# Optimization experiments

Hardware: AMD Instinct MI355X
Metric: run time of the kernel (lower is better)

The kernel has to match this reference:

```python
import jax, jax.numpy as jnp
import numpy as np

B, N = 4, 1024
IN_FEAT = 64
FNET = 64          # code requires fnet_feat == in_feat
OUT_FEAT = 64
RANK = 16
ST1 = 16
ST2 = 16
MIN_NN = 16


def _roll_idx(n_rolls, stride, F):
    # myroll(h, shift) == roll right by `shift` (mod F). Shifts used: 0, then (ss+1)*stride for ss=1..n_rolls-1.
    shifts = np.array([0] + [(ss + 1) * stride for ss in range(1, n_rolls)])
    j = np.arange(F)
    return jnp.asarray((j[None, :] - shifts[:, None]) % F)  # [n_rolls, F]


def setup_inputs() -> dict:
    key = jax.random.key(0)
    ks = jax.random.split(key, 10)
    h = jax.random.normal(ks[0], (B, N, IN_FEAT), jnp.float32)
    D = jax.random.uniform(ks[1], (B, N, N), jnp.float32)
    W0 = jax.random.normal(ks[2], (IN_FEAT, FNET), jnp.float32) * (1.0 / np.sqrt(IN_FEAT))
    b0 = jax.random.normal(ks[3], (1, FNET), jnp.float32) * 0.02
    W1 = jax.random.normal(ks[4], (FNET, ST1 * RANK), jnp.float32) * (1.0 / (np.sqrt(FNET) * np.sqrt(IN_FEAT)))
    b1 = jax.random.normal(ks[5], (1, RANK, IN_FEAT), jnp.float32) * 0.02
    W2 = jax.random.normal(ks[6], (FNET, ST2 * RANK), jnp.float32) * (1.0 / (np.sqrt(FNET) * np.sqrt(IN_FEAT)))
    b2 = jax.random.normal(ks[7], (1, RANK, OUT_FEAT), jnp.float32) * 0.02
    Wl = jax.random.normal(ks[8], (FNET, RANK), jnp.float32) * (1.0 / np.sqrt(RANK))
    bl = jax.random.normal(ks[9], (1, RANK), jnp.float32) * 0.02
    return {"h": h, "D": D, "W0": W0, "b0": b0, "W1": W1, "b1": b1,
            "W2": W2, "b2": b2, "Wl": Wl, "bl": bl}


def reference(h, D, W0, b0, W1, b1, W2, b2, Wl, bl):
    Bb, Nn, f = h.shape
    # k+1 nearest (smallest D): index 0 is the closest ('self'), 1..k are the neighbors
    _, top_idx = jax.lax.top_k(-D, MIN_NN + 1)            # [B, N, K+1]
    top_idx2 = jnp.repeat(top_idx[:, :, 0], MIN_NN, axis=1)  # [B, N*K] (repeat_interleave)
    nbr = top_idx[:, :, 1:].reshape(Bb, Nn * MIN_NN)         # [B, N*K]
    xt1 = jnp.take_along_axis(h, nbr[:, :, None], axis=1)    # [B, N*K, f]
    xt2 = jnp.take_along_axis(h, top_idx2[:, :, None], axis=1)
    labels = (xt1 - xt2).reshape(-1, f)                      # [E, f], E = B*N*K
    x1 = xt1.reshape(-1, f)
    d_labels = jnp.sum(labels * labels, axis=1).reshape(-1, MIN_NN)  # [B*N, K]
    lab = jax.nn.leaky_relu(labels @ W0 + b0, negative_slope=0.02)   # [E, FNET]
    E = lab.shape[0]
    idx1 = _roll_idx(IN_FEAT // ST1, ST1, FNET)
    idx2 = _roll_idx(OUT_FEAT // ST2, ST2, FNET)
    # per-edge weight generation via rolled copies of lab
    theta1 = (lab[:, idx1].reshape(-1, FNET) @ W1).reshape(E, RANK, IN_FEAT) + b1   # [E, R, in]
    theta2 = (lab[:, idx2].reshape(-1, FNET) @ W2).reshape(E, RANK, OUT_FEAT) + b2  # [E, R, out]
    thetal = lab @ Wl + bl                                                          # [E, R]
    x = jnp.einsum('erf,ef->er', theta1, x1) * thetal      # [E, R]
    x = jnp.einsum('ero,er->eo', theta2, x)                # [E, out]
    x = x.reshape(-1, MIN_NN, OUT_FEAT) * jnp.exp(-d_labels / 10.0)[:, :, None]
    x = jnp.sum(x, axis=1).reshape(-1, OUT_FEAT, Nn)       # faithful to torch .reshape(-1, out, N)
    return x
```

## Files before the change

kernel.cpp:

```cpp
#include <hip/hip_runtime.h>
#include <math.h>

#define NN 1024
#define K 16

typedef _Float16 f16;
typedef f16 f16x8 __attribute__((ext_vector_type(8)));
typedef float f32x4 __attribute__((ext_vector_type(4)));

typedef __attribute__((address_space(1))) void gvoid;
typedef __attribute__((address_space(3))) void svoid;

#define W0F_OFF 0
#define W1F_OFF 8192
#define W2F_OFF 40960
#define WLF_OFF 73728
#define B1F_OFF 75776
#define FRAG_BYTES 77824

#define MFMA16(a,b,c) __builtin_amdgcn_mfma_f32_16x16x32_f16((a),(b),(c),0,0,0)

template<int CTRL>
__device__ __forceinline__ float dppf(float v) {
    return __int_as_float(__builtin_amdgcn_update_dpp(0, __float_as_int(v), CTRL, 0xF, 0xF, true));
}
template<int CTRL>
__device__ __forceinline__ int dppi(int v) {
    return __builtin_amdgcn_update_dpp(0, v, CTRL, 0xF, 0xF, true);
}
__device__ __forceinline__ float rowsum16(float v) {
    v += dppf<0xB1>(v);
    v += dppf<0x4E>(v);
    v += dppf<0x124>(v);
    v += dppf<0x128>(v);
    return v;
}
__device__ __forceinline__ void argmin_step(float& bv, int& bidx, float ov, int oi) {
    bool t = (ov < bv) || (ov == bv && oi < bidx);
    bv = t ? ov : bv;
    bidx = t ? oi : bidx;
}

__global__ __launch_bounds__(256) void pre_kernel(const float* __restrict__ D,
                                                  const float* __restrict__ W0,
                                                  const float* __restrict__ W1,
                                                  const float* __restrict__ W2,
                                                  const float* __restrict__ Wl,
                                                  const float* __restrict__ b1,
                                                  int* __restrict__ selfIdx,
                                                  int* __restrict__ nbrIdx,
                                                  f16* __restrict__ frag) {
    if (blockIdx.x >= 1024) {
        int c = (blockIdx.x - 1024) * 256 + threadIdx.x;
        if (c >= 76 * 64) return;
        int fg   = c >> 6;
        int lane = c & 63;
        int lrow = lane & 15;
        int kgrp = lane >> 4;
        float src[8];
        if (fg < 8) {
            int kt = fg >> 2, nt = fg & 3;
            int n = nt * 16 + lrow;
#pragma unroll
            for (int i = 0; i < 8; ++i) src[i] = W0[(kt * 32 + kgrp * 8 + i) * 64 + n];
        } else if (fg < 40) {
            int t = fg - 8;
            int q = t >> 3, kt = (t >> 2) & 1, nt = t & 3;
            int f = nt * 16 + lrow;
#pragma unroll
            for (int i = 0; i < 8; ++i) src[i] = W1[f * 256 + q * 64 + kt * 32 + kgrp * 8 + i];
        } else if (fg < 72) {
            int t = fg - 40;
            int q = t >> 3, kt = (t >> 2) & 1, nt = t & 3;
            int o = nt * 16 + lrow;
#pragma unroll
            for (int i = 0; i < 8; ++i) src[i] = W2[(kt * 32 + kgrp * 8 + i) * 256 + q * 64 + o];
        } else if (fg < 74) {
            int kt = fg - 72;
#pragma unroll
            for (int i = 0; i < 8; ++i) src[i] = Wl[(kt * 32 + kgrp * 8 + i) * 16 + lrow];
        } else {
            int kt = fg - 74;
#pragma unroll
            for (int i = 0; i < 8; ++i) src[i] = b1[lrow * 64 + kt * 32 + kgrp * 8 + i];
        }
        f16x8 v;
#pragma unroll
        for (int i = 0; i < 8; ++i) v[i] = (f16)src[i];
        *(f16x8*)((unsigned char*)frag + fg * 1024 + lane * 16) = v;
        return;
    }

    int row  = blockIdx.x * 4 + (threadIdx.x >> 6);
    int lane = threadIdx.x & 63;
    const float* Drow = D + (size_t)row * NN + lane * 16;

    float v[16];
    {
        float4 t0 = *(const float4*)(Drow);
        float4 t1 = *(const float4*)(Drow + 4);
        float4 t2 = *(const float4*)(Drow + 8);
        float4 t3 = *(const float4*)(Drow + 12);
        v[0]=t0.x;  v[1]=t0.y;  v[2]=t0.z;  v[3]=t0.w;
        v[4]=t1.x;  v[5]=t1.y;  v[6]=t1.z;  v[7]=t1.w;
        v[8]=t2.x;  v[9]=t2.y;  v[10]=t2.z; v[11]=t2.w;
        v[12]=t3.x; v[13]=t3.y; v[14]=t3.z; v[15]=t3.w;
    }

    for (int t = 0; t < K + 1; ++t) {
        float bv = v[0]; int bj = 0;
#pragma unroll
        for (int j = 1; j < 16; ++j)
            if (v[j] < bv) { bv = v[j]; bj = j; }
        int bidx = lane * 16 + bj;
        argmin_step(bv, bidx, dppf<0xB1>(bv),  dppi<0xB1>(bidx));
        argmin_step(bv, bidx, dppf<0x4E>(bv),  dppi<0x4E>(bidx));
        argmin_step(bv, bidx, dppf<0x124>(bv), dppi<0x124>(bidx));
        argmin_step(bv, bidx, dppf<0x128>(bv), dppi<0x128>(bidx));
        argmin_step(bv, bidx, __shfl_xor(bv, 16), __shfl_xor(bidx, 16));
        argmin_step(bv, bidx, __shfl_xor(bv, 32), __shfl_xor(bidx, 32));

        if (lane == 0) {
            if (t == 0) selfIdx[row] = bidx;
            else        nbrIdx[row * K + (t - 1)] = bidx;
        }
        int hit = ((bidx >> 4) == lane) ? (bidx & 15) : 16;
#pragma unroll
        for (int j = 0; j < 16; ++j) v[j] = (j == hit) ? INFINITY : v[j];
    }
}

__global__ __launch_bounds__(1024, 4) void node_kernel(
    const float* __restrict__ h,
    const float* __restrict__ b0, const float* __restrict__ b2,
    const float* __restrict__ bl,
    const f16* __restrict__ frag,
    const int* __restrict__ selfIdx, const int* __restrict__ nbrIdx,
    float* __restrict__ out) {

    __shared__ __attribute__((aligned(16))) unsigned char sfrag[FRAG_BYTES];
    __shared__ __attribute__((aligned(16))) f16 sbuf[16 * 1152];
    __shared__ __attribute__((aligned(16))) float sxr[16 * 256];

    const int tid  = threadIdx.x;
    const int wid  = tid >> 6;
    const int lane = tid & 63;
    const int lrow = lane & 15;
    const int kgrp = lane >> 4;
    const int node = blockIdx.x * 16 + wid;

    {
        const unsigned char* gbase = (const unsigned char*)frag;
#pragma unroll
        for (int it = 0; it < 5; ++it) {
            int chunk = it * 1024 + wid * 64;
            if (chunk < 4864) {
                __builtin_amdgcn_global_load_lds(
                    (gvoid*)(gbase + (size_t)(chunk + lane) * 16),
                    (svoid*)(sfrag + (size_t)chunk * 16),
                    16, 0, 0);
            }
        }
    }

    const int self = selfIdx[node];
    const int nb   = nbrIdx[node * 16 + lrow];
    const float* hb = h + ((size_t)(node >> 10) << 16);

    f16x8 x1f[2], lrf[2];
    float dp = 0.f;
#pragma unroll
    for (int kt = 0; kt < 2; ++kt) {
        const float* p1 = hb + nb * 64 + kt * 32 + kgrp * 8;
        const float* p2 = hb + self * 64 + kt * 32 + kgrp * 8;
        float4 a0 = *(const float4*)(p1);
        float4 a1 = *(const float4*)(p1 + 4);
        float4 s0 = *(const float4*)(p2);
        float4 s1 = *(const float4*)(p2 + 4);
        float xs[8] = {a0.x,a0.y,a0.z,a0.w,a1.x,a1.y,a1.z,a1.w};
        float ss[8] = {s0.x,s0.y,s0.z,s0.w,s1.x,s1.y,s1.z,s1.w};
#pragma unroll
        for (int i = 0; i < 8; ++i) {
            float t = xs[i] - ss[i];
            x1f[kt][i] = (f16)xs[i];
            lrf[kt][i] = (f16)t;
            dp = fmaf(t, t, dp);
        }
    }
    dp += __shfl_xor(dp, 16);
    dp += __shfl_xor(dp, 32);
    const float dv = dp;

    __syncthreads();

    const unsigned char* fb = sfrag;
    f16* buf = sbuf + wid * 1152;
    float* xrbuf = sxr + wid * 256;

    f32x4 labf[4];
#pragma unroll
    for (int nt = 0; nt < 4; ++nt) {
        float bb = b0[nt * 16 + lrow];
        labf[nt] = (f32x4){bb, bb, bb, bb};
    }
#pragma unroll
    for (int kt = 0; kt < 2; ++kt)
#pragma unroll
        for (int nt = 0; nt < 4; ++nt) {
            f16x8 bf = *(const f16x8*)(fb + W0F_OFF + (kt * 4 + nt) * 1024 + lane * 16);
            labf[nt] = MFMA16(lrf[kt], bf, labf[nt]);
        }
#pragma unroll
    for (int nt = 0; nt < 4; ++nt)
#pragma unroll
        for (int j = 0; j < 4; ++j) {
            float v = labf[nt][j];
            v = v > 0.f ? v : 0.02f * v;
            labf[nt][j] = v;
            buf[(kgrp*4 + j) * 72 + nt*16 + lrow] = (f16)v;
        }

    f32x4 thlf, b1xf;
    {
        float blv = bl[lrow];
        thlf = (f32x4){blv, blv, blv, blv};
        b1xf = (f32x4){0.f, 0.f, 0.f, 0.f};
#pragma unroll
        for (int kt = 0; kt < 2; ++kt) {
            f16x8 wl = *(const f16x8*)(fb + WLF_OFF + kt * 1024 + lane * 16);
            f16x8 bb = *(const f16x8*)(fb + B1F_OFF + kt * 1024 + lane * 16);
            f16x8 la = *(const f16x8*)&buf[lrow * 72 + kt*32 + kgrp*8];
            thlf = MFMA16(la, wl, thlf);
            b1xf = MFMA16(x1f[kt], bb, b1xf);
        }
    }

    const int pown = lrow >> 2;
    f32x4 xof[4];
#pragma unroll
    for (int nt = 0; nt < 4; ++nt) xof[nt] = (f32x4){0.f, 0.f, 0.f, 0.f};

#pragma unroll
    for (int q = 0; q < 4; ++q) {
        f32x4 Uf[4];
#pragma unroll
        for (int nt = 0; nt < 4; ++nt) Uf[nt] = (f32x4){0.f, 0.f, 0.f, 0.f};
#pragma unroll
        for (int kt = 0; kt < 2; ++kt)
#pragma unroll
            for (int nt = 0; nt < 4; ++nt) {
                f16x8 bf = *(const f16x8*)(fb + W1F_OFF + (q*8 + kt*4 + nt) * 1024 + lane * 16);
                Uf[nt] = MFMA16(x1f[kt], bf, Uf[nt]);
            }

        f32x4 p0 = labf[0]*Uf[0] + labf[1]*Uf[1] + labf[2]*Uf[2] + labf[3]*Uf[3];
        f32x4 p1 = labf[0]*Uf[2] + labf[1]*Uf[3] + labf[2]*Uf[0] + labf[3]*Uf[1];
        f32x4 p2 = labf[0]*Uf[3] + labf[1]*Uf[0] + labf[2]*Uf[1] + labf[3]*Uf[2];
#pragma unroll
        for (int j = 0; j < 4; ++j) {
            p0[j] = rowsum16(p0[j]);
            p1[j] = rowsum16(p1[j]);
            p2[j] = rowsum16(p2[j]);
        }

        f32x4 dsel = (pown == 1) ? p1 : (pown == 2) ? p2 : p0;
        f32x4 cand = (dsel + b1xf) * thlf;
        *(f32x4*)(xrbuf + lrow * 16 + kgrp * 4) = cand;

        f32x4 xr[4];
#pragma unroll
        for (int p = 0; p < 4; ++p)
            xr[p] = *(const f32x4*)(xrbuf + (p * 4 + q) * 16 + kgrp * 4);

        {
            f32x4 x03 = xr[0] + xr[3];
#pragma unroll
            for (int nt = 0; nt < 4; ++nt) {
                f32x4 v = labf[nt] * x03
                        + labf[(nt + 2) & 3] * xr[1]
                        + labf[(nt + 1) & 3] * xr[2];
#pragma unroll
                for (int j = 0; j < 4; ++j)
                    buf[(kgrp*4 + j) * 72 + nt*16 + lrow] = (f16)v[j];
            }
        }

#pragma unroll
        for (int kt = 0; kt < 2; ++kt) {
            f16x8 av = *(const f16x8*)&buf[lrow * 72 + kt*32 + kgrp*8];
#pragma unroll
            for (int nt = 0; nt < 4; ++nt) {
                f16x8 bf = *(const f16x8*)(fb + W2F_OFF + (q*8 + kt*4 + nt) * 1024 + lane * 16);
                xof[nt] = MFMA16(av, bf, xof[nt]);
            }
        }

#pragma unroll
        for (int p = 0; p < 4; ++p)
#pragma unroll
            for (int nt = 0; nt < 4; ++nt) {
                float bv = b2[(p*4 + q) * 64 + nt*16 + lrow];
                xof[nt] += xr[p] * bv;
            }
    }

    f32x4 ew;
#pragma unroll
    for (int j = 0; j < 4; ++j) {
        float dd = __shfl(dv, kgrp * 4 + j);
        ew[j] = __expf(-dd * 0.1f);
    }
    float cs[4];
#pragma unroll
    for (int nt = 0; nt < 4; ++nt) {
        f32x4 wp = xof[nt] * ew;
        float s = wp[0] + wp[1] + wp[2] + wp[3];
        s += __shfl_xor(s, 16);
        s += __shfl_xor(s, 32);
        cs[nt] = s;
    }
    float v = (kgrp == 0) ? cs[0] : (kgrp == 1) ? cs[1] : (kgrp == 2) ? cs[2] : cs[3];
    out[(size_t)node * 64 + lane] = v;
}

extern "C" void kernel_launch(void* const* d_in, const int* in_sizes, int n_in,
                              void* d_out, int out_size, void* d_ws, size_t ws_size,
                              hipStream_t stream) {
    const float* h  = (const float*)d_in[0];
    const float* D  = (const float*)d_in[1];
    const float* W0 = (const float*)d_in[2];
    const float* b0 = (const float*)d_in[3];
    const float* W1 = (const float*)d_in[4];
    const float* b1 = (const float*)d_in[5];
    const float* W2 = (const float*)d_in[6];
    const float* b2 = (const float*)d_in[7];
    const float* Wl = (const float*)d_in[8];
    const float* bl = (const float*)d_in[9];
    float* out = (float*)d_out;

    int* selfIdx = (int*)d_ws;
    int* nbrIdx  = selfIdx + 4096;
    f16* frag    = (f16*)(nbrIdx + 65536);

    pre_kernel<<<1043, 256, 0, stream>>>(D, W0, W1, W2, Wl, b1,
                                         selfIdx, nbrIdx, frag);
    node_kernel<<<256, 1024, 0, stream>>>(h, b0, b2, bl, frag,
                                          selfIdx, nbrIdx, out);
}
```

Baseline: 40.28 us.

## Process two nodes per wavefront to reuse weight fragments across MFMAs

Each wavefront now handles two nodes instead of one, halving the block size to 512 threads while keeping 16 nodes per block. Every weight fragment read from shared memory now feeds two MFMAs, which is meant to halve LDS traffic per node and give more independent MFMA work to interleave. In exchange register pressure roughly doubles, the launch bounds drop to 512 threads, and with fewer waves per block there is less latency hiding.

```diff
diff --git a/kernel.cpp b/kernel.cpp
--- a/kernel.cpp
+++ b/kernel.cpp
@@ -130,7 +130,7 @@
     }
 }
 
-__global__ __launch_bounds__(1024, 4) void node_kernel(
+__global__ __launch_bounds__(512, 2) void node_kernel(
     const float* __restrict__ h,
     const float* __restrict__ b0, const float* __restrict__ b2,
     const float* __restrict__ bl,
@@ -147,13 +147,13 @@
     const int lane = tid & 63;
     const int lrow = lane & 15;
     const int kgrp = lane >> 4;
-    const int node = blockIdx.x * 16 + wid;
+    const int n0   = blockIdx.x * 16 + wid * 2;
 
     {
         const unsigned char* gbase = (const unsigned char*)frag;
 #pragma unroll
-        for (int it = 0; it < 5; ++it) {
-            int chunk = it * 1024 + wid * 64;
+        for (int it = 0; it < 10; ++it) {
+            int chunk = it * 512 + wid * 64;
             if (chunk < 4864) {
                 __builtin_amdgcn_global_load_lds(
                     (gvoid*)(gbase + (size_t)(chunk + lane) * 16),
@@ -163,122 +163,154 @@
         }
     }
 
-    const int self = selfIdx[node];
-    const int nb   = nbrIdx[node * 16 + lrow];
-    const float* hb = h + ((size_t)(node >> 10) << 16);
-
-    f16x8 x1f[2], lrf[2];
-    float dp = 0.f;
-#pragma unroll
-    for (int kt = 0; kt < 2; ++kt) {
-        const float* p1 = hb + nb * 64 + kt * 32 + kgrp * 8;
-        const float* p2 = hb + self * 64 + kt * 32 + kgrp * 8;
-        float4 a0 = *(const float4*)(p1);
-        float4 a1 = *(const float4*)(p1 + 4);
-        float4 s0 = *(const float4*)(p2);
-        float4 s1 = *(const float4*)(p2 + 4);
-        float xs[8] = {a0.x,a0.y,a0.z,a0.w,a1.x,a1.y,a1.z,a1.w};
-        float ss[8] = {s0.x,s0.y,s0.z,s0.w,s1.x,s1.y,s1.z,s1.w};
-#pragma unroll
-        for (int i = 0; i < 8; ++i) {
-            float t = xs[i] - ss[i];
-            x1f[kt][i] = (f16)xs[i];
-            lrf[kt][i] = (f16)t;
-            dp = fmaf(t, t, dp);
-        }
-    }
-    dp += __shfl_xor(dp, 16);
-    dp += __shfl_xor(dp, 32);
-    const float dv = dp;
+    const float* hb = h + ((size_t)(n0 >> 10) << 16);
+
+    f16x8 x1f[2][2], lrf[2][2];
+    float dv[2];
+#pragma unroll
+    for (int mt = 0; mt < 2; ++mt) {
+        const int node = n0 + mt;
+        const int self = selfIdx[node];
+        const int nb   = nbrIdx[node * 16 + lrow];
+        float dp = 0.f;
+#pragma unroll
+        for (int kt = 0; kt < 2; ++kt) {
+            const float* p1 = hb + nb * 64 + kt * 32 + kgrp * 8;
+            const float* p2 = hb + self * 64 + kt * 32 + kgrp * 8;
+            float4 a0 = *(const float4*)(p1);
+            float4 a1 = *(const float4*)(p1 + 4);
+            float4 s0 = *(const float4*)(p2);
+            float4 s1 = *(const float4*)(p2 + 4);
+            float xs[8] = {a0.x,a0.y,a0.z,a0.w,a1.x,a1.y,a1.z,a1.w};
+            float ss[8] = {s0.x,s0.y,s0.z,s0.w,s1.x,s1.y,s1.z,s1.w};
+#pragma unroll
+            for (int i = 0; i < 8; ++i) {
+                float t = xs[i] - ss[i];
+                x1f[mt][kt][i] = (f16)xs[i];
+                lrf[mt][kt][i] = (f16)t;
+                dp = fmaf(t, t, dp);
+            }
+        }
+        dp += __shfl_xor(dp, 16);
+        dp += __shfl_xor(dp, 32);
+        dv[mt] = dp;
+    }
 
     __syncthreads();
 
     const unsigned char* fb = sfrag;
-    f16* buf = sbuf + wid * 1152;
-    float* xrbuf = sxr + wid * 256;
-
-    f32x4 labf[4];
+    f16* buf0 = sbuf + (wid * 2 + 0) * 1152;
+    f16* buf1 = sbuf + (wid * 2 + 1) * 1152;
+    float* xrb0 = sxr + (wid * 2 + 0) * 256;
+    float* xrb1 = sxr + (wid * 2 + 1) * 256;
+
+    f32x4 labf[2][4];
 #pragma unroll
     for (int nt = 0; nt < 4; ++nt) {
         float bb = b0[nt * 16 + lrow];
-        labf[nt] = (f32x4){bb, bb, bb, bb};
+        labf[0][nt] = (f32x4){bb, bb, bb, bb};
+        labf[1][nt] = labf[0][nt];
     }
 #pragma unroll
     for (int kt = 0; kt < 2; ++kt)
 #pragma unroll
         for (int nt = 0; nt < 4; ++nt) {
             f16x8 bf = *(const f16x8*)(fb + W0F_OFF + (kt * 4 + nt) * 1024 + lane * 16);
-            labf[nt] = MFMA16(lrf[kt], bf, labf[nt]);
+            labf[0][nt] = MFMA16(lrf[0][kt], bf, labf[0][nt]);
+            labf[1][nt] = MFMA16(lrf[1][kt], bf, labf[1][nt]);
         }
 #pragma unroll
     for (int nt = 0; nt < 4; ++nt)
 #pragma unroll
         for (int j = 0; j < 4; ++j) {
-            float v = labf[nt][j];
-            v = v > 0.f ? v : 0.02f * v;
-            labf[nt][j] = v;
-            buf[(kgrp*4 + j) * 72 + nt*16 + lrow] = (f16)v;
-        }
-
-    f32x4 thlf, b1xf;
+            float v0 = labf[0][nt][j];
+            float v1 = labf[1][nt][j];
+            v0 = v0 > 0.f ? v0 : 0.02f * v0;
+            v1 = v1 > 0.f ? v1 : 0.02f * v1;
+            labf[0][nt][j] = v0;
+            labf[1][nt][j] = v1;
+            buf0[(kgrp*4 + j) * 72 + nt*16 + lrow] = (f16)v0;
+            buf1[(kgrp*4 + j) * 72 + nt*16 + lrow] = (f16)v1;
+        }
+
+    f32x4 thlf[2], b1xf[2];
     {
         float blv = bl[lrow];
-        thlf = (f32x4){blv, blv, blv, blv};
-        b1xf = (f32x4){0.f, 0.f, 0.f, 0.f};
+        thlf[0] = (f32x4){blv, blv, blv, blv};
+        thlf[1] = thlf[0];
+        b1xf[0] = (f32x4){0.f, 0.f, 0.f, 0.f};
+        b1xf[1] = b1xf[0];
 #pragma unroll
         for (int kt = 0; kt < 2; ++kt) {
             f16x8 wl = *(const f16x8*)(fb + WLF_OFF + kt * 1024 + lane * 16);
             f16x8 bb = *(const f16x8*)(fb + B1F_OFF + kt * 1024 + lane * 16);
-            f16x8 la = *(const f16x8*)&buf[lrow * 72 + kt*32 + kgrp*8];
-            thlf = MFMA16(la, wl, thlf);
-            b1xf = MFMA16(x1f[kt], bb, b1xf);
+            f16x8 la0 = *(const f16x8*)&buf0[lrow * 72 + kt*32 + kgrp*8];
+            f16x8 la1 = *(const f16x8*)&buf1[lrow * 72 + kt*32 + kgrp*8];
+            thlf[0] = MFMA16(la0, wl, thlf[0]);
+            thlf[1] = MFMA16(la1, wl, thlf[1]);
+            b1xf[0] = MFMA16(x1f[0][kt], bb, b1xf[0]);
+            b1xf[1] = MFMA16(x1f[1][kt], bb, b1xf[1]);
         }
     }
 
     const int pown = lrow >> 2;
-    f32x4 xof[4];
-#pragma unroll
-    for (int nt = 0; nt < 4; ++nt) xof[nt] = (f32x4){0.f, 0.f, 0.f, 0.f};
+    f32x4 xof[2][4];
+#pragma unroll
+    for (int nt = 0; nt < 4; ++nt) {
+        xof[0][nt] = (f32x4){0.f, 0.f, 0.f, 0.f};
+        xof[1][nt] = xof[0][nt];
+    }
 
 #pragma unroll
     for (int q = 0; q < 4; ++q) {
-        f32x4 Uf[4];
-#pragma unroll
-        for (int nt = 0; nt < 4; ++nt) Uf[nt] = (f32x4){0.f, 0.f, 0.f, 0.f};
+        f32x4 Uf[2][4];
+#pragma unroll
+        for (int nt = 0; nt < 4; ++nt) {
+            Uf[0][nt] = (f32x4){0.f, 0.f, 0.f, 0.f};
+            Uf[1][nt] = Uf[0][nt];
+        }
 #pragma unroll
         for (int kt = 0; kt < 2; ++kt)
 #pragma unroll
             for (int nt = 0; nt < 4; ++nt) {
                 f16x8 bf = *(const f16x8*)(fb + W1F_OFF + (q*8 + kt*4 + nt) * 1024 + lane * 16);
-                Uf[nt] = MFMA16(x1f[kt], bf, Uf[nt]);
-            }
-
-        f32x4 p0 = labf[0]*Uf[0] + labf[1]*Uf[1] + labf[2]*Uf[2] + labf[3]*Uf[3];
-        f32x4 p1 = labf[0]*Uf[2] + labf[1]*Uf[3] + labf[2]*Uf[0] + labf[3]*Uf[1];
-        f32x4 p2 = labf[0]*Uf[3] + labf[1]*Uf[0] + labf[2]*Uf[1] + labf[3]*Uf[2];
-#pragma unroll
-        for (int j = 0; j < 4; ++j) {
-            p0[j] = rowsum16(p0[j]);
-            p1[j] = rowsum16(p1[j]);
-            p2[j] = rowsum16(p2[j]);
-        }
-
-        f32x4 dsel = (pown == 1) ? p1 : (pown == 2) ? p2 : p0;
-        f32x4 cand = (dsel + b1xf) * thlf;
-        *(f32x4*)(xrbuf + lrow * 16 + kgrp * 4) = cand;
-
-        f32x4 xr[4];
-#pragma unroll
-        for (int p = 0; p < 4; ++p)
-            xr[p] = *(const f32x4*)(xrbuf + (p * 4 + q) * 16 + kgrp * 4);
-
-        {
-            f32x4 x03 = xr[0] + xr[3];
+                Uf[0][nt] = MFMA16(x1f[0][kt], bf, Uf[0][nt]);
+                Uf[1][nt] = MFMA16(x1f[1][kt], bf, Uf[1][nt]);
+            }
+
+        f32x4 xr[2][4];
+#pragma unroll
+        for (int mt = 0; mt < 2; ++mt) {
+            f32x4 p0 = labf[mt][0]*Uf[mt][0] + labf[mt][1]*Uf[mt][1]
+                     + labf[mt][2]*Uf[mt][2] + labf[mt][3]*Uf[mt][3];
+            f32x4 p1 = labf[mt][0]*Uf[mt][2] + labf[mt][1]*Uf[mt][3]
+                     + labf[mt][2]*Uf[mt][0] + labf[mt][3]*Uf[mt][1];
+            f32x4 p2 = labf[mt][0]*Uf[mt][3] + labf[mt][1]*Uf[mt][0]
+                     + labf[mt][2]*Uf[mt][1] + labf[mt][3]*Uf[mt][2];
+#pragma unroll
+            for (int j = 0; j < 4; ++j) {
+                p0[j] = rowsum16(p0[j]);
+                p1[j] = rowsum16(p1[j]);
+                p2[j] = rowsum16(p2[j]);
+            }
+            f32x4 dsel = (pown == 1) ? p1 : (pown == 2) ? p2 : p0;
+            f32x4 cand = (dsel + b1xf[mt]) * thlf[mt];
+            float* xrb = (mt == 0) ? xrb0 : xrb1;
+            *(f32x4*)(xrb + lrow * 16 + kgrp * 4) = cand;
+#pragma unroll
+            for (int p = 0; p < 4; ++p)
+                xr[mt][p] = *(const f32x4*)(xrb + (p * 4 + q) * 16 + kgrp * 4);
+        }
+
+#pragma unroll
+        for (int mt = 0; mt < 2; ++mt) {
+            f16* buf = (mt == 0) ? buf0 : buf1;
+            f32x4 x03 = xr[mt][0] + xr[mt][3];
 #pragma unroll
             for (int nt = 0; nt < 4; ++nt) {
-                f32x4 v = labf[nt] * x03
-                        + labf[(nt + 2) & 3] * xr[1]
-                        + labf[(nt + 1) & 3] * xr[2];
+                f32x4 v = labf[mt][nt] * x03
+                        + labf[mt][(nt + 2) & 3] * xr[mt][1]
+                        + labf[mt][(nt + 1) & 3] * xr[mt][2];
 #pragma unroll
                 for (int j = 0; j < 4; ++j)
                     buf[(kgrp*4 + j) * 72 + nt*16 + lrow] = (f16)v[j];
@@ -287,11 +319,13 @@
 
 #pragma unroll
         for (int kt = 0; kt < 2; ++kt) {
-            f16x8 av = *(const f16x8*)&buf[lrow * 72 + kt*32 + kgrp*8];
+            f16x8 av0 = *(const f16x8*)&buf0[lrow * 72 + kt*32 + kgrp*8];
+            f16x8 av1 = *(const f16x8*)&buf1[lrow * 72 + kt*32 + kgrp*8];
 #pragma unroll
             for (int nt = 0; nt < 4; ++nt) {
                 f16x8 bf = *(const f16x8*)(fb + W2F_OFF + (q*8 + kt*4 + nt) * 1024 + lane * 16);
-                xof[nt] = MFMA16(av, bf, xof[nt]);
+                xof[0][nt] = MFMA16(av0, bf, xof[0][nt]);
+                xof[1][nt] = MFMA16(av1, bf, xof[1][nt]);
             }
         }
 
@@ -300,27 +334,31 @@
 #pragma unroll
             for (int nt = 0; nt < 4; ++nt) {
                 float bv = b2[(p*4 + q) * 64 + nt*16 + lrow];
-                xof[nt] += xr[p] * bv;
-            }
-    }
-
-    f32x4 ew;
-#pragma unroll
-    for (int j = 0; j < 4; ++j) {
-        float dd = __shfl(dv, kgrp * 4 + j);
-        ew[j] = __expf(-dd * 0.1f);
-    }
-    float cs[4];
-#pragma unroll
-    for (int nt = 0; nt < 4; ++nt) {
-        f32x4 wp = xof[nt] * ew;
-        float s = wp[0] + wp[1] + wp[2] + wp[3];
-        s += __shfl_xor(s, 16);
-        s += __shfl_xor(s, 32);
-        cs[nt] = s;
-    }
-    float v = (kgrp == 0) ? cs[0] : (kgrp == 1) ? cs[1] : (kgrp == 2) ? cs[2] : cs[3];
-    out[(size_t)node * 64 + lane] = v;
+                xof[0][nt] += xr[0][p] * bv;
+                xof[1][nt] += xr[1][p] * bv;
+            }
+    }
+
+#pragma unroll
+    for (int mt = 0; mt < 2; ++mt) {
+        f32x4 ew;
+#pragma unroll
+        for (int j = 0; j < 4; ++j) {
+            float dd = __shfl(dv[mt], kgrp * 4 + j);
+            ew[j] = __expf(-dd * 0.1f);
+        }
+        float cs[4];
+#pragma unroll
+        for (int nt = 0; nt < 4; ++nt) {
+            f32x4 wp = xof[mt][nt] * ew;
+            float s = wp[0] + wp[1] + wp[2] + wp[3];
+            s += __shfl_xor(s, 16);
+            s += __shfl_xor(s, 32);
+            cs[nt] = s;
+        }
+        float v = (kgrp == 0) ? cs[0] : (kgrp == 1) ? cs[1] : (kgrp == 2) ? cs[2] : cs[3];
+        out[(size_t)(n0 + mt) * 64 + lane] = v;
+    }
 }
 
 extern "C" void kernel_launch(void* const* d_in, const int* in_sizes, int n_in,
@@ -344,6 +382,6 @@
 
     pre_kernel<<<1043, 256, 0, stream>>>(D, W0, W1, W2, Wl, b1,
                                          selfIdx, nbrIdx, frag);
-    node_kernel<<<256, 1024, 0, stream>>>(h, b0, b2, bl, frag,
-                                          selfIdx, nbrIdx, out);
-}
+    node_kernel<<<256, 512, 0, stream>>>(h, b0, b2, bl, frag,
+                                         selfIdx, nbrIdx, out);
+}
```

Measured after the change: 40.39 us. About the same (+0.3%).
